# Optimization experiments

Measured on AMD Instinct MI355X. Metric: run time of the kernel, lower is better.

The kernel has to match this reference:

```python
import jax, jax.numpy as jnp
import numpy as np

EPS = 1e-6
N_SRC = 100000
N_TAR = 100000
N = N_SRC + N_TAR
DIM = 128
E = 600000
NEG_SLOPE = 0.01  # torch leaky_relu default


def setup_inputs() -> dict:
    key = jax.random.key(0)
    ks = jax.random.split(key, 8)
    x_src = jax.random.normal(ks[0], (N_SRC, DIM), dtype=jnp.float32)
    x_tar = jax.random.normal(ks[1], (N_TAR, DIM), dtype=jnp.float32)
    edge_index = jax.random.randint(ks[2], (2, E), 0, N, dtype=jnp.int64)
    edge_weight = jax.random.uniform(ks[3], (E,), dtype=jnp.float32)
    W_gcn = jax.random.normal(ks[4], (DIM, DIM), dtype=jnp.float32) / np.sqrt(DIM)
    b_gcn = jax.random.normal(ks[5], (DIM,), dtype=jnp.float32) * 0.01
    W_fnn = jax.random.normal(ks[6], (DIM, DIM), dtype=jnp.float32) / np.sqrt(DIM)
    b_fnn = jax.random.normal(ks[7], (DIM,), dtype=jnp.float32) * 0.01
    return dict(x_src=x_src, x_tar=x_tar, edge_index=edge_index,
                edge_weight=edge_weight, W_gcn=W_gcn, b_gcn=b_gcn,
                W_fnn=W_fnn, b_fnn=b_fnn)


def _gcn_conv(x, edge_index, edge_weight, W, b):
    # PyG GCNConv with add_self_loops=True, symmetric normalization.
    row = jnp.concatenate([edge_index[0], jnp.arange(N, dtype=edge_index.dtype)])
    col = jnp.concatenate([edge_index[1], jnp.arange(N, dtype=edge_index.dtype)])
    w = jnp.concatenate([edge_weight, jnp.ones((N,), dtype=edge_weight.dtype)])
    deg = jax.ops.segment_sum(w, col, num_segments=N)
    dinv = jnp.where(deg > 0, jax.lax.rsqrt(deg), 0.0)
    norm = dinv[row] * w * dinv[col]                 # [E+N]
    h = x @ W                                        # [N, D]
    msg = norm[:, None] * h[row]                     # gather + scale
    out = jnp.zeros_like(h).at[col].add(msg)         # scatter-add to targets
    return out + b


def _node_norm(x):
    mean = jnp.mean(x, axis=1, keepdims=True)
    var = jnp.mean((x - mean) ** 2, axis=1, keepdims=True)  # unbiased=False
    return (x - mean) / jnp.sqrt(var + EPS)


def reference(x_src, x_tar, edge_index, edge_weight, W_gcn, b_gcn, W_fnn, b_fnn):
    x = jnp.concatenate([x_src, x_tar], axis=0)      # [N, D]
    # route == 'MIX': GNN branch + FNN branch on the skip copy
    g = _gcn_conv(x, edge_index, edge_weight, W_gcn, b_gcn)
    f = jax.nn.leaky_relu(x @ W_fnn + b_fnn, NEG_SLOPE)  # dropout = identity (eval)
    x = g + f
    x = _node_norm(x)
    x = jax.nn.leaky_relu(x, NEG_SLOPE)
    return x[:N_SRC, :], x[N_SRC:, :]
```

## Files before the change

### kernel.cpp

```cpp
#include <hip/hip_runtime.h>
#include <hip/hip_bf16.h>
#include <cstddef>
#include <cstdint>

#define DIM 128
#define SCAN_CHUNK 2048

typedef __attribute__((ext_vector_type(8))) short short8v;
typedef __attribute__((ext_vector_type(4))) float f32x4;

__device__ __forceinline__ float leaky(float v) {
    return v > 0.0f ? v : 0.01f * v;
}

__device__ __forceinline__ unsigned short f2bf(float f) {
    unsigned u = __builtin_bit_cast(unsigned, f);
    u += 0x7FFF + ((u >> 16) & 1);
    return (unsigned short)(u >> 16);
}

__device__ __forceinline__ unsigned cvt_pk_bf16(float a, float b) {
    unsigned r;
    asm("v_cvt_pk_bf16_f32 %0, %1, %2" : "=v"(r) : "v"(a), "v"(b));
    return r;
}

__device__ __forceinline__ float bf2f_hi(unsigned p) {
    return __builtin_bit_cast(float, p & 0xFFFF0000u);
}
__device__ __forceinline__ float bf2f_lo(unsigned p) {
    return __builtin_bit_cast(float, p << 16);
}

__global__ __launch_bounds__(256)
void init_kernel(const float* __restrict__ Wg, const float* __restrict__ Wf,
                 unsigned short* __restrict__ WgT, unsigned short* __restrict__ WfT,
                 int* __restrict__ cnt, int N) {
    int t = blockIdx.x * 256 + threadIdx.x;
    if (t < N) cnt[t] = 0;
    if (t < 128 * 128) {
        int col = t >> 7, k = t & 127;
        WgT[col * 128 + k] = f2bf(Wg[k * 128 + col]);
        WfT[col * 128 + k] = f2bf(Wf[k * 128 + col]);
    }
}

__global__ __launch_bounds__(256)
void hist_kernel(const int* __restrict__ col, int* __restrict__ cnt, int E) {
    int e = blockIdx.x * blockDim.x + threadIdx.x;
    if (e < E) atomicAdd(&cnt[col[e]], 1);
}

__global__ __launch_bounds__(256)
void scan_block_sums(const int* __restrict__ cnt, int* __restrict__ bsum, int N) {
    __shared__ int sdata[4];
    int base = blockIdx.x * SCAN_CHUNK;
    int s = 0;
    for (int k = threadIdx.x; k < SCAN_CHUNK; k += 256) {
        int idx = base + k;
        s += (idx < N) ? cnt[idx] : 0;
    }
#pragma unroll
    for (int m = 1; m < 64; m <<= 1) s += __shfl_xor(s, m, 64);
    if ((threadIdx.x & 63) == 0) sdata[threadIdx.x >> 6] = s;
    __syncthreads();
    if (threadIdx.x == 0)
        bsum[blockIdx.x] = sdata[0] + sdata[1] + sdata[2] + sdata[3];
}

__global__ __launch_bounds__(128)
void scan_bsum_kernel(int* __restrict__ bsum, int nb) {
    __shared__ int wtot[2];
    int t = threadIdx.x;
    int lane = t & 63;
    int orig = (t < nb) ? bsum[t] : 0;
    int v = orig;
#pragma unroll
    for (int m = 1; m < 64; m <<= 1) {
        int u = __shfl_up(v, m, 64);
        if (lane >= m) v += u;
    }
    if (lane == 63) wtot[t >> 6] = v;
    __syncthreads();
    if (t >= 64) v += wtot[0];
    if (t < nb) bsum[t] = v - orig;
}

__global__ __launch_bounds__(256)
void scan_write_kernel(int* __restrict__ cnt, const int* __restrict__ bsum,
                       int* __restrict__ off, int N) {
    __shared__ int wsum[4];
    int t = threadIdx.x;
    int base = blockIdx.x * SCAN_CHUNK + t * 8;
    int vals[8];
    int local = 0;
#pragma unroll
    for (int k = 0; k < 8; ++k) {
        int idx = base + k;
        int c = (idx < N) ? cnt[idx] : 0;
        vals[k] = local;
        local += c;
    }
    int tsum = local;
    int lane = t & 63;
    int v = tsum;
#pragma unroll
    for (int m = 1; m < 64; m <<= 1) {
        int u = __shfl_up(v, m, 64);
        if (lane >= m) v += u;
    }
    if (lane == 63) wsum[t >> 6] = v;
    __syncthreads();
    int woff = 0;
    for (int i = 0; i < (t >> 6); ++i) woff += wsum[i];
    int texcl = (v - tsum) + woff + bsum[blockIdx.x];
#pragma unroll
    for (int k = 0; k < 8; ++k) {
        int idx = base + k;
        int o = texcl + vals[k];
        if (idx <= N) off[idx] = o;
    }
    __syncthreads();
#pragma unroll
    for (int k = 0; k < 8; ++k) {
        int idx = base + k;
        int o = texcl + vals[k];
        if (idx < N) cnt[idx] = o;
    }
}

__global__ __launch_bounds__(256)
void reorder_kernel(const int* __restrict__ row, const int* __restrict__ col,
                    const float* __restrict__ w, int* __restrict__ cursor,
                    int2* __restrict__ edgeRW, int E) {
    int e = blockIdx.x * blockDim.x + threadIdx.x;
    if (e < E) {
        int c = col[e];
        int pos = atomicAdd(&cursor[c], 1);
        edgeRW[pos] = make_int2(row[e], __builtin_bit_cast(int, w[e]));
    }
}

__global__ __launch_bounds__(256)
void csr_dinv_kernel(const int* __restrict__ off, const int2* __restrict__ edgeRW,
                     float* __restrict__ dinv, int N) {
    int i = blockIdx.x * 256 + threadIdx.x;
    if (i >= N) return;
    int s = off[i], e = off[i + 1];
    float acc = 1.0f;
    for (int j = s; j < e; ++j)
        acc += __builtin_bit_cast(float, edgeRW[j].y);
    dinv[i] = rsqrtf(acc);
}

__global__ __launch_bounds__(512, 4)
void gemm_mfma_kernel(const float* __restrict__ x_src, const float* __restrict__ x_tar,
                      int n_src, int n_total,
                      const unsigned short* __restrict__ WgT,
                      const unsigned short* __restrict__ WfT,
                      const float* __restrict__ bg, const float* __restrict__ bf,
                      const float* __restrict__ dinv,
                      unsigned short* __restrict__ hsb,
                      unsigned short* __restrict__ accb)
{
    __shared__ unsigned short Ash[128 * 128];

    const int t = threadIdx.x;

#pragma unroll
    for (int s = 0; s < 4; ++s) {
        int id  = t + s * 512;
        int row = id >> 4;
        int c   = id & 15;
        int rg  = blockIdx.x * 128 + row;
        if (rg > n_total - 1) rg = n_total - 1;
        const float* xr = (rg < n_src) ? x_src + (size_t)rg * DIM
                                       : x_tar + (size_t)(rg - n_src) * DIM;
        float4 v0 = *(const float4*)(xr + c * 8);
        float4 v1 = *(const float4*)(xr + c * 8 + 4);
        union { uint4 q; unsigned short us[8]; } cv;
        cv.us[0] = f2bf(v0.x); cv.us[1] = f2bf(v0.y);
        cv.us[2] = f2bf(v0.z); cv.us[3] = f2bf(v0.w);
        cv.us[4] = f2bf(v1.x); cv.us[5] = f2bf(v1.y);
        cv.us[6] = f2bf(v1.z); cv.us[7] = f2bf(v1.w);
        *(uint4*)&Ash[(size_t)row * 128 + ((c ^ (row & 15)) * 8)] = cv.q;
    }
    __syncthreads();

    const int lane = t & 63;
    const int wave = t >> 6;
    const int wr = wave >> 2;
    const int wc = wave & 3;
    const int lr = lane & 15;
    const int lk = lane >> 4;

    f32x4 accg[4][2], accf[4][2];
#pragma unroll
    for (int i = 0; i < 4; ++i)
#pragma unroll
        for (int j = 0; j < 2; ++j) {
            accg[i][j] = (f32x4)0.0f;
            accf[i][j] = (f32x4)0.0f;
        }

#pragma unroll
    for (int ks = 0; ks < 4; ++ks) {
        short8v xf[4];
#pragma unroll
        for (int mf = 0; mf < 4; ++mf) {
            int row = wr * 64 + mf * 16 + lr;
            int cc  = ks * 4 + lk;
            xf[mf] = *(const short8v*)&Ash[(size_t)row * 128 + ((cc ^ (row & 15)) * 8)];
        }
#pragma unroll
        for (int nf = 0; nf < 2; ++nf) {
            int col = wc * 32 + nf * 16 + lr;
            const size_t bo = (size_t)col * 128 + ks * 32 + lk * 8;
            short8v bgv = *(const short8v*)(WgT + bo);
            short8v bfv = *(const short8v*)(WfT + bo);
#pragma unroll
            for (int mf = 0; mf < 4; ++mf) {
                accg[mf][nf] = __builtin_amdgcn_mfma_f32_16x16x32_bf16(bgv, xf[mf], accg[mf][nf], 0, 0, 0);
                accf[mf][nf] = __builtin_amdgcn_mfma_f32_16x16x32_bf16(bfv, xf[mf], accf[mf][nf], 0, 0, 0);
            }
        }
    }

#pragma unroll
    for (int mf = 0; mf < 4; ++mf) {
        int r = blockIdx.x * 128 + wr * 64 + mf * 16 + lr;
        const bool valid = (r < n_total);
        int rc = valid ? r : (n_total - 1);
        float dv = dinv[rc];
#pragma unroll
        for (int nf = 0; nf < 2; ++nf) {
            int c0 = wc * 32 + nf * 16 + lk * 4;
            float4 bgv = *(const float4*)(bg + c0);
            float4 bfv = *(const float4*)(bf + c0);

            float hs0 = dv * accg[mf][nf][0];
            float hs1 = dv * accg[mf][nf][1];
            float hs2 = dv * accg[mf][nf][2];
            float hs3 = dv * accg[mf][nf][3];

            float o0 = leaky(accf[mf][nf][0] + bfv.x) + bgv.x + dv * hs0;
            float o1 = leaky(accf[mf][nf][1] + bfv.y) + bgv.y + dv * hs1;
            float o2 = leaky(accf[mf][nf][2] + bfv.z) + bgv.z + dv * hs2;
            float o3 = leaky(accf[mf][nf][3] + bfv.w) + bgv.w + dv * hs3;

            uint2 hp, op;
            hp.x = cvt_pk_bf16(hs0, hs1);
            hp.y = cvt_pk_bf16(hs2, hs3);
            op.x = cvt_pk_bf16(o0, o1);
            op.y = cvt_pk_bf16(o2, o3);

            if (valid) {
                *(uint2*)(hsb  + (size_t)r * DIM + c0) = hp;
                *(uint2*)(accb + (size_t)r * DIM + c0) = op;
            }
        }
    }
}

__global__ __launch_bounds__(256)
void gather_norm_kernel(const int* __restrict__ off, const int2* __restrict__ edgeRW,
                        const float* __restrict__ dinv,
                        const unsigned short* __restrict__ hsb,
                        const unsigned short* __restrict__ accb,
                        float* __restrict__ out, int n)
{
    const int wid  = threadIdx.x >> 6;
    const int lane = threadIdx.x & 63;
    const int sub  = lane >> 4;
    const int sl   = lane & 15;
    int i = (blockIdx.x * 4 + wid) * 4 + sub;
    if (i >= n) i = n - 1;

    const int start = off[i];
    const int degc  = off[i + 1] - start;

    int md = degc;
    md = max(md, __shfl_xor(md, 16, 64));
    md = max(md, __shfl_xor(md, 32, 64));

    float s[8];
#pragma unroll
    for (int k = 0; k < 8; ++k) s[k] = 0.0f;

    const unsigned short* gbase = hsb + (size_t)sl * 8;

    int   r0 = 0, r1 = 0;
    float w0 = 0.0f, w1 = 0.0f;
    if (0 < degc) { int2 m = edgeRW[start];     r0 = m.x; w0 = __builtin_bit_cast(float, m.y); }
    if (1 < degc) { int2 m = edgeRW[start + 1]; r1 = m.x; w1 = __builtin_bit_cast(float, m.y); }
    uint4 p0 = *(const uint4*)(gbase + (size_t)r0 * DIM);

    for (int t = 0; t < md; ++t) {
        uint4 p1 = p0;
        if (t + 1 < md)
            p1 = *(const uint4*)(gbase + (size_t)r1 * DIM);
        int r2 = 0; float w2 = 0.0f;
        if (t + 2 < md) {
            if (t + 2 < degc) {
                int2 m = edgeRW[start + t + 2];
                r2 = m.x; w2 = __builtin_bit_cast(float, m.y);
            }
        }
        s[0] += w0 * bf2f_lo(p0.x); s[1] += w0 * bf2f_hi(p0.x);
        s[2] += w0 * bf2f_lo(p0.y); s[3] += w0 * bf2f_hi(p0.y);
        s[4] += w0 * bf2f_lo(p0.z); s[5] += w0 * bf2f_hi(p0.z);
        s[6] += w0 * bf2f_lo(p0.w); s[7] += w0 * bf2f_hi(p0.w);
        p0 = p1;
        r0 = r1; w0 = w1;
        r1 = r2; w1 = w2;
    }

    const float dv = dinv[i];
    uint4 av = *(const uint4*)(accb + (size_t)i * DIM + sl * 8);
    float v[8];
    v[0] = bf2f_lo(av.x) + dv * s[0]; v[1] = bf2f_hi(av.x) + dv * s[1];
    v[2] = bf2f_lo(av.y) + dv * s[2]; v[3] = bf2f_hi(av.y) + dv * s[3];
    v[4] = bf2f_lo(av.z) + dv * s[4]; v[5] = bf2f_hi(av.z) + dv * s[5];
    v[6] = bf2f_lo(av.w) + dv * s[6]; v[7] = bf2f_hi(av.w) + dv * s[7];

    float sum = 0.0f;
#pragma unroll
    for (int k = 0; k < 8; ++k) sum += v[k];
#pragma unroll
    for (int m = 1; m < 16; m <<= 1) sum += __shfl_xor(sum, m, 64);
    const float mean = sum * (1.0f / 128.0f);

    float sq = 0.0f;
#pragma unroll
    for (int k = 0; k < 8; ++k) {
        v[k] -= mean;
        sq += v[k] * v[k];
    }
#pragma unroll
    for (int m = 1; m < 16; m <<= 1) sq += __shfl_xor(sq, m, 64);
    const float rstd = rsqrtf(sq * (1.0f / 128.0f) + 1e-6f);

    float4 o1, o2;
    o1.x = leaky(v[0] * rstd); o1.y = leaky(v[1] * rstd);
    o1.z = leaky(v[2] * rstd); o1.w = leaky(v[3] * rstd);
    o2.x = leaky(v[4] * rstd); o2.y = leaky(v[5] * rstd);
    o2.z = leaky(v[6] * rstd); o2.w = leaky(v[7] * rstd);
    float* op = out + (size_t)i * DIM + sl * 8;
    *(float4*)op       = o1;
    *(float4*)(op + 4) = o2;
}

extern "C" void kernel_launch(void* const* d_in, const int* in_sizes, int n_in,
                              void* d_out, int out_size, void* d_ws, size_t ws_size,
                              hipStream_t stream)
{
    const float* x_src = (const float*)d_in[0];
    const float* x_tar = (const float*)d_in[1];
    const int*   ei    = (const int*)d_in[2];
    const float* ew    = (const float*)d_in[3];
    const float* Wg    = (const float*)d_in[4];
    const float* bg    = (const float*)d_in[5];
    const float* Wf    = (const float*)d_in[6];
    const float* bf    = (const float*)d_in[7];

    const int n_src = in_sizes[0] / DIM;
    const int n_tar = in_sizes[1] / DIM;
    const int N     = n_src + n_tar;
    const int E     = in_sizes[3];

    const int* rowp = ei;
    const int* colp = ei + E;

    char* p = (char*)d_ws;
    float* dinv = (float*)p;  p += (size_t)N * 4;
    int*   cnt  = (int*)p;    p += (size_t)N * 4;
    int*   off  = (int*)p;    p += (size_t)(N + 1) * 4;
    int*   bsum = (int*)p;    p += 160 * 4;
    p = (char*)(((uintptr_t)p + 15) & ~(uintptr_t)15);
    int2*  edgeRW = (int2*)p; p += (size_t)E * 8;
    unsigned short* hsb  = (unsigned short*)p; p += (size_t)N * DIM * 2;
    unsigned short* accb = (unsigned short*)p; p += (size_t)N * DIM * 2;
    unsigned short* WgT  = (unsigned short*)p; p += 128 * 128 * 2;
    unsigned short* WfT  = (unsigned short*)p;

    const int NB = (N + 1 + SCAN_CHUNK - 1) / SCAN_CHUNK;

    init_kernel<<<(N + 255) / 256, 256, 0, stream>>>(Wg, Wf, WgT, WfT, cnt, N);

    hist_kernel<<<(E + 255) / 256, 256, 0, stream>>>(colp, cnt, E);

    scan_block_sums<<<NB, 256, 0, stream>>>(cnt, bsum, N);
    scan_bsum_kernel<<<1, 128, 0, stream>>>(bsum, NB);
    scan_write_kernel<<<NB, 256, 0, stream>>>(cnt, bsum, off, N);

    reorder_kernel<<<(E + 255) / 256, 256, 0, stream>>>(rowp, colp, ew, cnt,
                                                        edgeRW, E);

    csr_dinv_kernel<<<(N + 255) / 256, 256, 0, stream>>>(off, edgeRW, dinv, N);

    gemm_mfma_kernel<<<(N + 127) / 128, 512, 0, stream>>>(
        x_src, x_tar, n_src, N, WgT, WfT, bg, bf, dinv, hsb, accb);

    gather_norm_kernel<<<(N + 15) / 16, 256, 0, stream>>>(
        off, edgeRW, dinv, hsb, accb, (float*)d_out, N);
}
```

Measured before the change: 216.3 us.

## Drop LDS staging in GEMM; each wave loads its own 16 rows directly

The MFMA GEMM no longer stages a 128-row bf16 tile of x in shared memory behind a block barrier. Each wave now loads its own 16 rows straight from global memory, converts them to bf16 in registers, and computes all 128 output columns for both weight matrices. Blocks shrink to 256 threads covering 64 rows. This removes the LDS round trip and the __syncthreads, but weight fragments are reused across fewer rows per load, so weight traffic from cache rises and each wave holds more accumulators.

```diff
diff --git a/kernel.cpp b/kernel.cpp
--- a/kernel.cpp
+++ b/kernel.cpp
@@ -153,7 +153,7 @@
     dinv[i] = rsqrtf(acc);
 }
 
-__global__ __launch_bounds__(512, 4)
+__global__ __launch_bounds__(256, 4)
 void gemm_mfma_kernel(const float* __restrict__ x_src, const float* __restrict__ x_tar,
                       int n_src, int n_total,
                       const unsigned short* __restrict__ WgT,
@@ -163,101 +163,73 @@
                       unsigned short* __restrict__ hsb,
                       unsigned short* __restrict__ accb)
 {
-    __shared__ unsigned short Ash[128 * 128];
-
-    const int t = threadIdx.x;
-
-#pragma unroll
-    for (int s = 0; s < 4; ++s) {
-        int id  = t + s * 512;
-        int row = id >> 4;
-        int c   = id & 15;
-        int rg  = blockIdx.x * 128 + row;
-        if (rg > n_total - 1) rg = n_total - 1;
-        const float* xr = (rg < n_src) ? x_src + (size_t)rg * DIM
-                                       : x_tar + (size_t)(rg - n_src) * DIM;
-        float4 v0 = *(const float4*)(xr + c * 8);
-        float4 v1 = *(const float4*)(xr + c * 8 + 4);
-        union { uint4 q; unsigned short us[8]; } cv;
-        cv.us[0] = f2bf(v0.x); cv.us[1] = f2bf(v0.y);
-        cv.us[2] = f2bf(v0.z); cv.us[3] = f2bf(v0.w);
-        cv.us[4] = f2bf(v1.x); cv.us[5] = f2bf(v1.y);
-        cv.us[6] = f2bf(v1.z); cv.us[7] = f2bf(v1.w);
-        *(uint4*)&Ash[(size_t)row * 128 + ((c ^ (row & 15)) * 8)] = cv.q;
-    }
-    __syncthreads();
-
+    const int t    = threadIdx.x;
     const int lane = t & 63;
     const int wave = t >> 6;
-    const int wr = wave >> 2;
-    const int wc = wave & 3;
-    const int lr = lane & 15;
-    const int lk = lane >> 4;
-
-    f32x4 accg[4][2], accf[4][2];
-#pragma unroll
-    for (int i = 0; i < 4; ++i)
-#pragma unroll
-        for (int j = 0; j < 2; ++j) {
-            accg[i][j] = (f32x4)0.0f;
-            accf[i][j] = (f32x4)0.0f;
-        }
+    const int lr   = lane & 15;
+    const int lk   = lane >> 4;
+
+    const int rb  = (blockIdx.x * 4 + wave) * 16;
+    int row = rb + lr;
+    const bool valid = (row < n_total);
+    int rc = valid ? row : (n_total - 1);
+    const float* xr = (rc < n_src) ? x_src + (size_t)rc * DIM
+                                   : x_tar + (size_t)(rc - n_src) * DIM;
+
+    f32x4 accg[8], accf[8];
+#pragma unroll
+    for (int nf = 0; nf < 8; ++nf) {
+        accg[nf] = (f32x4)0.0f;
+        accf[nf] = (f32x4)0.0f;
+    }
 
 #pragma unroll
     for (int ks = 0; ks < 4; ++ks) {
-        short8v xf[4];
-#pragma unroll
-        for (int mf = 0; mf < 4; ++mf) {
-            int row = wr * 64 + mf * 16 + lr;
-            int cc  = ks * 4 + lk;
-            xf[mf] = *(const short8v*)&Ash[(size_t)row * 128 + ((cc ^ (row & 15)) * 8)];
-        }
-#pragma unroll
-        for (int nf = 0; nf < 2; ++nf) {
-            int col = wc * 32 + nf * 16 + lr;
+        float4 xa = *(const float4*)(xr + ks * 32 + lk * 8);
+        float4 xb = *(const float4*)(xr + ks * 32 + lk * 8 + 4);
+        union { short8v v; unsigned u[4]; } xf;
+        xf.u[0] = cvt_pk_bf16(xa.x, xa.y);
+        xf.u[1] = cvt_pk_bf16(xa.z, xa.w);
+        xf.u[2] = cvt_pk_bf16(xb.x, xb.y);
+        xf.u[3] = cvt_pk_bf16(xb.z, xb.w);
+
+#pragma unroll
+        for (int nf = 0; nf < 8; ++nf) {
+            int col = nf * 16 + lr;
             const size_t bo = (size_t)col * 128 + ks * 32 + lk * 8;
             short8v bgv = *(const short8v*)(WgT + bo);
             short8v bfv = *(const short8v*)(WfT + bo);
-#pragma unroll
-            for (int mf = 0; mf < 4; ++mf) {
-                accg[mf][nf] = __builtin_amdgcn_mfma_f32_16x16x32_bf16(bgv, xf[mf], accg[mf][nf], 0, 0, 0);
-                accf[mf][nf] = __builtin_amdgcn_mfma_f32_16x16x32_bf16(bfv, xf[mf], accf[mf][nf], 0, 0, 0);
-            }
+            accg[nf] = __builtin_amdgcn_mfma_f32_16x16x32_bf16(bgv, xf.v, accg[nf], 0, 0, 0);
+            accf[nf] = __builtin_amdgcn_mfma_f32_16x16x32_bf16(bfv, xf.v, accf[nf], 0, 0, 0);
         }
     }
 
-#pragma unroll
-    for (int mf = 0; mf < 4; ++mf) {
-        int r = blockIdx.x * 128 + wr * 64 + mf * 16 + lr;
-        const bool valid = (r < n_total);
-        int rc = valid ? r : (n_total - 1);
-        float dv = dinv[rc];
-#pragma unroll
-        for (int nf = 0; nf < 2; ++nf) {
-            int c0 = wc * 32 + nf * 16 + lk * 4;
-            float4 bgv = *(const float4*)(bg + c0);
-            float4 bfv = *(const float4*)(bf + c0);
-
-            float hs0 = dv * accg[mf][nf][0];
-            float hs1 = dv * accg[mf][nf][1];
-            float hs2 = dv * accg[mf][nf][2];
-            float hs3 = dv * accg[mf][nf][3];
-
-            float o0 = leaky(accf[mf][nf][0] + bfv.x) + bgv.x + dv * hs0;
-            float o1 = leaky(accf[mf][nf][1] + bfv.y) + bgv.y + dv * hs1;
-            float o2 = leaky(accf[mf][nf][2] + bfv.z) + bgv.z + dv * hs2;
-            float o3 = leaky(accf[mf][nf][3] + bfv.w) + bgv.w + dv * hs3;
-
-            uint2 hp, op;
-            hp.x = cvt_pk_bf16(hs0, hs1);
-            hp.y = cvt_pk_bf16(hs2, hs3);
-            op.x = cvt_pk_bf16(o0, o1);
-            op.y = cvt_pk_bf16(o2, o3);
-
-            if (valid) {
-                *(uint2*)(hsb  + (size_t)r * DIM + c0) = hp;
-                *(uint2*)(accb + (size_t)r * DIM + c0) = op;
-            }
+    const float dv = dinv[rc];
+#pragma unroll
+    for (int nf = 0; nf < 8; ++nf) {
+        int c0 = nf * 16 + lk * 4;
+        float4 bgv = *(const float4*)(bg + c0);
+        float4 bfv = *(const float4*)(bf + c0);
+
+        float hs0 = dv * accg[nf][0];
+        float hs1 = dv * accg[nf][1];
+        float hs2 = dv * accg[nf][2];
+        float hs3 = dv * accg[nf][3];
+
+        float o0 = leaky(accf[nf][0] + bfv.x) + bgv.x + dv * hs0;
+        float o1 = leaky(accf[nf][1] + bfv.y) + bgv.y + dv * hs1;
+        float o2 = leaky(accf[nf][2] + bfv.z) + bgv.z + dv * hs2;
+        float o3 = leaky(accf[nf][3] + bfv.w) + bgv.w + dv * hs3;
+
+        uint2 hp, op;
+        hp.x = cvt_pk_bf16(hs0, hs1);
+        hp.y = cvt_pk_bf16(hs2, hs3);
+        op.x = cvt_pk_bf16(o0, o1);
+        op.y = cvt_pk_bf16(o2, o3);
+
+        if (valid) {
+            *(uint2*)(hsb  + (size_t)row * DIM + c0) = hp;
+            *(uint2*)(accb + (size_t)row * DIM + c0) = op;
         }
     }
 }
@@ -398,7 +370,7 @@
 
     csr_dinv_kernel<<<(N + 255) / 256, 256, 0, stream>>>(off, edgeRW, dinv, N);
 
-    gemm_mfma_kernel<<<(N + 127) / 128, 512, 0, stream>>>(
+    gemm_mfma_kernel<<<(N + 63) / 64, 256, 0, stream>>>(
         x_src, x_tar, n_src, N, WgT, WfT, bg, bf, dinv, hsb, accb);
 
     gather_norm_kernel<<<(N + 15) / 16, 256, 0, stream>>>(
```

Result: slower. 287.9 us (+33.1%).
